# Performance work log

Measured on AMD Instinct MI355X. Metric: run time of the kernel, lower is better.

## Reference

```python
import jax, jax.numpy as jnp
import numpy as np

B, S, D = 64, 2048, 512


def setup_inputs() -> dict:
    key = jax.random.key(0)
    k1, k2, k3, k4 = jax.random.split(key, 4)
    decoder_output = jax.random.normal(k1, (B, 1, D), dtype=jnp.float32)
    encoder_output = jax.random.normal(k2, (B, S, D), dtype=jnp.float32)
    # W_a_tanh: Dense(D) applied to concat([dec, enc]) of width 2D
    scale_w = 1.0 / np.sqrt(2 * D)
    W_t = jax.random.normal(k3, (2 * D, D), dtype=jnp.float32) * scale_w
    b_t = jnp.zeros((D,), dtype=jnp.float32)
    # v_a: Dense(1)
    v_a = jax.random.normal(k4, (D, 1), dtype=jnp.float32) * (1.0 / np.sqrt(D))
    b_v = jnp.zeros((1,), dtype=jnp.float32)
    return {
        "decoder_output": decoder_output,
        "encoder_output": encoder_output,
        "W_t": W_t,
        "b_t": b_t,
        "v_a": v_a,
        "b_v": b_v,
    }


def reference(decoder_output, encoder_output, W_t, b_t, v_a, b_v):
    # concat-variant Luong attention
    dec = jnp.broadcast_to(decoder_output, encoder_output.shape)       # [B,S,D]
    concated = jnp.concatenate((dec, encoder_output), axis=-1)          # [B,S,2D]
    hidden = jnp.tanh(jnp.einsum('bse,ed->bsd', concated, W_t) + b_t)   # [B,S,D]
    score = (jnp.einsum('bsd,do->bso', hidden, v_a) + b_v)              # [B,S,1]
    score = jnp.transpose(score, (0, 2, 1))                             # [B,1,S]
    alignment_vector = jax.nn.softmax(score, axis=2)                    # [B,1,S]
    context_vector = jnp.matmul(alignment_vector, encoder_output)       # [B,1,D]
    return (context_vector, alignment_vector)
```

## Files before the change

### kernel.cpp

```cpp
#include <hip/hip_runtime.h>
#include <hip/hip_bf16.h>

#define BB 64
#define SS 2048
#define DD 512
#define MM (BB * SS)

typedef __attribute__((ext_vector_type(8))) short bf16x8;
typedef __attribute__((ext_vector_type(4))) float f32x4;

__device__ __forceinline__ unsigned f2bf(float f) {
    unsigned u = __float_as_uint(f);
    u += 0x7FFFu + ((u >> 16) & 1u);
    return u >> 16;
}

__device__ __forceinline__ float fast_tanh(float x) {
    float ax = fabsf(x);
    float e = __expf(-2.0f * ax);
    float t = (1.0f - e) * __builtin_amdgcn_rcpf(1.0f + e);
    return x < 0.0f ? -t : t;
}

__global__ void prep_w(const float* __restrict__ W, short* __restrict__ Bt) {
    __shared__ float tile[64][65];
    int kt = blockIdx.x >> 3;
    int nt = blockIdx.x & 7;
    int t = threadIdx.x;
    int c = t & 63;
    int rbase = (t >> 6) * 16;
    #pragma unroll
    for (int i = 0; i < 16; ++i) {
        int r = rbase + i;
        tile[r][c] = W[(size_t)(512 + kt * 64 + r) * DD + nt * 64 + c];
    }
    __syncthreads();
    #pragma unroll
    for (int i = 0; i < 16; ++i) {
        int r = rbase + i;
        Bt[(size_t)(nt * 64 + r) * DD + kt * 64 + c] = (short)f2bf(tile[c][r]);
    }
}

__global__ void prep_p(const float* __restrict__ dec, const float* __restrict__ W,
                       const float* __restrict__ bt, float* __restrict__ p) {
    int b = blockIdx.x;
    int d = blockIdx.y * 256 + threadIdx.x;
    float acc = bt[d];
    const float* dv = dec + (size_t)b * DD;
    #pragma unroll 8
    for (int e = 0; e < DD; ++e)
        acc += dv[e] * W[(size_t)e * DD + d];
    p[(size_t)b * DD + d] = acc;
}

__global__ __launch_bounds__(256, 2)
void score_gemm(const float* __restrict__ enc,
                const short* __restrict__ Bt,
                const float* __restrict__ p,
                const float* __restrict__ va,
                float* __restrict__ score) {
    __shared__ short Alds[2][128 * 32];
    __shared__ short Blds[2][128 * 32];
    __shared__ float sp[4][64];

    const int tid  = threadIdx.x;
    const int wave = tid >> 6;
    const int lane = tid & 63;
    const int mblk = blockIdx.x >> 2;
    const int n0   = (blockIdx.x & 3) * 128;
    const int m0   = mblk * 128;

    const int wm = wave >> 1, wn = wave & 1;
    const int lm = lane & 15, lq = lane >> 4;

    f32x4 acc[4][4];
    #pragma unroll
    for (int i = 0; i < 4; ++i)
        #pragma unroll
        for (int j = 0; j < 4; ++j)
            acc[i][j] = (f32x4){0.f, 0.f, 0.f, 0.f};

    const int arow = tid >> 1;
    const int acol = (tid & 1) * 16;
    const float* aptr = enc + (size_t)(m0 + arow) * DD + acol;

    const short* bptr = Bt + (size_t)(n0 + wave * 32 + (lane >> 2)) * DD + (lane & 3) * 8;

    #pragma unroll
    for (int i = 0; i < 2; ++i)
        __builtin_amdgcn_global_load_lds(
            (const __attribute__((address_space(1))) void*)(bptr + (size_t)i * 16 * DD),
            (__attribute__((address_space(3))) void*)(&Blds[0][(wave * 32 + i * 16) * 32]),
            16, 0, 0);
    {
        f32x4 x0 = *(const f32x4*)(aptr);
        f32x4 x1 = *(const f32x4*)(aptr + 4);
        f32x4 x2 = *(const f32x4*)(aptr + 8);
        f32x4 x3 = *(const f32x4*)(aptr + 12);
        int4 p0, p1;
        p0.x = f2bf(x0.x) | (f2bf(x0.y) << 16);
        p0.y = f2bf(x0.z) | (f2bf(x0.w) << 16);
        p0.z = f2bf(x1.x) | (f2bf(x1.y) << 16);
        p0.w = f2bf(x1.z) | (f2bf(x1.w) << 16);
        p1.x = f2bf(x2.x) | (f2bf(x2.y) << 16);
        p1.y = f2bf(x2.z) | (f2bf(x2.w) << 16);
        p1.z = f2bf(x3.x) | (f2bf(x3.y) << 16);
        p1.w = f2bf(x3.z) | (f2bf(x3.w) << 16);
        *(int4*)(&Alds[0][arow * 32 + acol]) = p0;
        *(int4*)(&Alds[0][arow * 32 + acol + 8]) = p1;
    }
    __syncthreads();

    for (int kt = 0; kt < 16; ++kt) {
        const int c = kt & 1;
        const bool pf = kt < 15;
        f32x4 x0, x1, x2, x3;
        if (pf) {
            const int kn = (kt + 1) * 32;
            #pragma unroll
            for (int i = 0; i < 2; ++i)
                __builtin_amdgcn_global_load_lds(
                    (const __attribute__((address_space(1))) void*)(bptr + (size_t)i * 16 * DD + kn),
                    (__attribute__((address_space(3))) void*)(&Blds[1 - c][(wave * 32 + i * 16) * 32]),
                    16, 0, 0);
            x0 = *(const f32x4*)(aptr + kn);
            x1 = *(const f32x4*)(aptr + kn + 4);
            x2 = *(const f32x4*)(aptr + kn + 8);
            x3 = *(const f32x4*)(aptr + kn + 12);
        }
        bf16x8 af[4];
        #pragma unroll
        for (int mf = 0; mf < 4; ++mf)
            af[mf] = *(const bf16x8*)(&Alds[c][(wm * 64 + mf * 16 + lm) * 32 + lq * 8]);
        #pragma unroll
        for (int nf = 0; nf < 4; ++nf) {
            bf16x8 bfr = *(const bf16x8*)(&Blds[c][(wn * 64 + nf * 16 + lm) * 32 + lq * 8]);
            #pragma unroll
            for (int mf = 0; mf < 4; ++mf)
                acc[mf][nf] = __builtin_amdgcn_mfma_f32_16x16x32_bf16(af[mf], bfr, acc[mf][nf], 0, 0, 0);
        }
        if (pf) {
            int4 p0, p1;
            p0.x = f2bf(x0.x) | (f2bf(x0.y) << 16);
            p0.y = f2bf(x0.z) | (f2bf(x0.w) << 16);
            p0.z = f2bf(x1.x) | (f2bf(x1.y) << 16);
            p0.w = f2bf(x1.z) | (f2bf(x1.w) << 16);
            p1.x = f2bf(x2.x) | (f2bf(x2.y) << 16);
            p1.y = f2bf(x2.z) | (f2bf(x2.w) << 16);
            p1.z = f2bf(x3.x) | (f2bf(x3.y) << 16);
            p1.w = f2bf(x3.z) | (f2bf(x3.w) << 16);
            *(int4*)(&Alds[1 - c][arow * 32 + acol]) = p0;
            *(int4*)(&Alds[1 - c][arow * 32 + acol + 8]) = p1;
        }
        __syncthreads();
    }

    const int b = m0 >> 11;
    float rowsum[4][4];
    #pragma unroll
    for (int mf = 0; mf < 4; ++mf)
        #pragma unroll
        for (int r = 0; r < 4; ++r) rowsum[mf][r] = 0.f;

    #pragma unroll
    for (int nf = 0; nf < 4; ++nf) {
        int n = n0 + wn * 64 + nf * 16 + lm;
        float pv = p[(size_t)b * DD + n];
        float vv = va[n];
        #pragma unroll
        for (int mf = 0; mf < 4; ++mf)
            #pragma unroll
            for (int r = 0; r < 4; ++r)
                rowsum[mf][r] += fast_tanh(pv + acc[mf][nf][r]) * vv;
    }
    #pragma unroll
    for (int mf = 0; mf < 4; ++mf)
        #pragma unroll
        for (int r = 0; r < 4; ++r) {
            float s = rowsum[mf][r];
            s += __shfl_xor(s, 1);
            s += __shfl_xor(s, 2);
            s += __shfl_xor(s, 4);
            s += __shfl_xor(s, 8);
            rowsum[mf][r] = s;
        }
    if (lm == 0) {
        #pragma unroll
        for (int mf = 0; mf < 4; ++mf)
            #pragma unroll
            for (int r = 0; r < 4; ++r)
                sp[wave][mf * 16 + lq * 4 + r] = rowsum[mf][r];
    }
    __syncthreads();
    if (tid < 128) {
        int row = tid & 63, half = tid >> 6;
        float v = sp[half * 2][row] + sp[half * 2 + 1][row];
        atomicAdd(&score[(size_t)m0 + half * 64 + row], v);
    }
}

__global__ void softmax_k(const float* __restrict__ score, float* __restrict__ align) {
    __shared__ float red[256];
    int b = blockIdx.x, tid = threadIdx.x;
    const float* s = score + (size_t)b * SS;
    float vals[8];
    float mx = -1e30f;
    #pragma unroll
    for (int i = 0; i < 8; ++i) {
        vals[i] = s[i * 256 + tid];
        mx = fmaxf(mx, vals[i]);
    }
    red[tid] = mx; __syncthreads();
    for (int off = 128; off > 0; off >>= 1) {
        if (tid < off) red[tid] = fmaxf(red[tid], red[tid + off]);
        __syncthreads();
    }
    mx = red[0]; __syncthreads();
    float sum = 0.f;
    #pragma unroll
    for (int i = 0; i < 8; ++i) {
        vals[i] = __expf(vals[i] - mx);
        sum += vals[i];
    }
    red[tid] = sum; __syncthreads();
    for (int off = 128; off > 0; off >>= 1) {
        if (tid < off) red[tid] += red[tid + off];
        __syncthreads();
    }
    float inv = 1.0f / red[0];
    #pragma unroll
    for (int i = 0; i < 8; ++i)
        align[(size_t)b * SS + i * 256 + tid] = vals[i] * inv;
}

__global__ void context_k(const float* __restrict__ enc, const float* __restrict__ align,
                          float* __restrict__ ctx) {
    int bx = blockIdx.x;
    int b = bx >> 4, chunk = bx & 15;
    int tid = threadIdx.x;
    const float2* e2 = (const float2*)(enc + ((size_t)b * SS + chunk * 128) * DD);
    const float* a = align + (size_t)b * SS + chunk * 128;
    float2 acc = {0.f, 0.f};
    #pragma unroll 4
    for (int s = 0; s < 128; ++s) {
        float av = a[s];
        float2 e = e2[(size_t)s * 256 + tid];
        acc.x += av * e.x;
        acc.y += av * e.y;
    }
    atomicAdd(&ctx[(size_t)b * DD + tid * 2], acc.x);
    atomicAdd(&ctx[(size_t)b * DD + tid * 2 + 1], acc.y);
}

extern "C" void kernel_launch(void* const* d_in, const int* in_sizes, int n_in,
                              void* d_out, int out_size, void* d_ws, size_t ws_size,
                              hipStream_t stream) {
    const float* dec = (const float*)d_in[0];
    const float* enc = (const float*)d_in[1];
    const float* W   = (const float*)d_in[2];
    const float* bt  = (const float*)d_in[3];
    const float* va  = (const float*)d_in[4];

    float* out   = (float*)d_out;
    float* ctx   = out;
    float* align = out + BB * DD;

    char*  ws    = (char*)d_ws;
    short* Bt    = (short*)ws;
    float* p     = (float*)(ws + 512 * 512 * 2);
    float* score = (float*)(ws + 512 * 512 * 2 + BB * DD * 4);

    hipMemsetAsync(ctx, 0, BB * DD * sizeof(float), stream);
    hipMemsetAsync(score, 0, MM * sizeof(float), stream);
    prep_w<<<64, 256, 0, stream>>>(W, Bt);
    prep_p<<<dim3(BB, 2), 256, 0, stream>>>(dec, W, bt, p);
    score_gemm<<<MM / 32, 256, 0, stream>>>(enc, Bt, p, va, score);
    softmax_k<<<BB, 256, 0, stream>>>(score, align);
    context_k<<<BB * 16, 256, 0, stream>>>(enc, align, ctx);
}
```

Measured before the change: 538.0 us.

## Pre-convert encoder to bf16 and stream both GEMM operands via direct LDS loads

Adds a separate pass that converts the fp32 encoder output to bf16 in workspace. The score GEMM then loads both A and B tiles with global_load_lds double buffering instead of per-thread fp32 loads, conversion and LDS stores, and raises the occupancy hint to 4 blocks per CU. The trade is an extra full read of the fp32 encoder plus a bf16 write and re-read (about 128 MB of extra traffic) in exchange for a leaner GEMM main loop. It also needs a large workspace, with a fallback to the old fp32 kernel when the workspace is too small.

```diff
diff --git a/kernel.cpp b/kernel.cpp
--- a/kernel.cpp
+++ b/kernel.cpp
@@ -20,6 +20,18 @@
     float e = __expf(-2.0f * ax);
     float t = (1.0f - e) * __builtin_amdgcn_rcpf(1.0f + e);
     return x < 0.0f ? -t : t;
+}
+
+__global__ void cvt_enc(const float* __restrict__ enc, short* __restrict__ enc16) {
+    size_t i = ((size_t)blockIdx.x * 256 + threadIdx.x) * 8;
+    f32x4 a = *(const f32x4*)(enc + i);
+    f32x4 b = *(const f32x4*)(enc + i + 4);
+    int4 pk;
+    pk.x = f2bf(a.x) | (f2bf(a.y) << 16);
+    pk.y = f2bf(a.z) | (f2bf(a.w) << 16);
+    pk.z = f2bf(b.x) | (f2bf(b.y) << 16);
+    pk.w = f2bf(b.z) | (f2bf(b.w) << 16);
+    *(int4*)(enc16 + i) = pk;
 }
 
 __global__ void prep_w(const float* __restrict__ W, short* __restrict__ Bt) {
@@ -54,8 +66,8 @@
     p[(size_t)b * DD + d] = acc;
 }
 
-__global__ __launch_bounds__(256, 2)
-void score_gemm(const float* __restrict__ enc,
+__global__ __launch_bounds__(256, 4)
+void score_gemm(const short* __restrict__ enc16,
                 const short* __restrict__ Bt,
                 const float* __restrict__ p,
                 const float* __restrict__ va,
@@ -81,10 +93,126 @@
         for (int j = 0; j < 4; ++j)
             acc[i][j] = (f32x4){0.f, 0.f, 0.f, 0.f};
 
+    const short* aptr = enc16 + (size_t)(m0 + wave * 32 + (lane >> 2)) * DD + (lane & 3) * 8;
+    const short* bptr = Bt    + (size_t)(n0 + wave * 32 + (lane >> 2)) * DD + (lane & 3) * 8;
+
+    #pragma unroll
+    for (int i = 0; i < 2; ++i) {
+        __builtin_amdgcn_global_load_lds(
+            (const __attribute__((address_space(1))) void*)(aptr + (size_t)i * 16 * DD),
+            (__attribute__((address_space(3))) void*)(&Alds[0][(wave * 32 + i * 16) * 32]),
+            16, 0, 0);
+        __builtin_amdgcn_global_load_lds(
+            (const __attribute__((address_space(1))) void*)(bptr + (size_t)i * 16 * DD),
+            (__attribute__((address_space(3))) void*)(&Blds[0][(wave * 32 + i * 16) * 32]),
+            16, 0, 0);
+    }
+    __syncthreads();
+
+    for (int kt = 0; kt < 16; ++kt) {
+        const int c = kt & 1;
+        if (kt < 15) {
+            const int kn = (kt + 1) * 32;
+            #pragma unroll
+            for (int i = 0; i < 2; ++i) {
+                __builtin_amdgcn_global_load_lds(
+                    (const __attribute__((address_space(1))) void*)(aptr + (size_t)i * 16 * DD + kn),
+                    (__attribute__((address_space(3))) void*)(&Alds[1 - c][(wave * 32 + i * 16) * 32]),
+                    16, 0, 0);
+                __builtin_amdgcn_global_load_lds(
+                    (const __attribute__((address_space(1))) void*)(bptr + (size_t)i * 16 * DD + kn),
+                    (__attribute__((address_space(3))) void*)(&Blds[1 - c][(wave * 32 + i * 16) * 32]),
+                    16, 0, 0);
+            }
+        }
+        bf16x8 af[4];
+        #pragma unroll
+        for (int mf = 0; mf < 4; ++mf)
+            af[mf] = *(const bf16x8*)(&Alds[c][(wm * 64 + mf * 16 + lm) * 32 + lq * 8]);
+        #pragma unroll
+        for (int nf = 0; nf < 4; ++nf) {
+            bf16x8 bfr = *(const bf16x8*)(&Blds[c][(wn * 64 + nf * 16 + lm) * 32 + lq * 8]);
+            #pragma unroll
+            for (int mf = 0; mf < 4; ++mf)
+                acc[mf][nf] = __builtin_amdgcn_mfma_f32_16x16x32_bf16(af[mf], bfr, acc[mf][nf], 0, 0, 0);
+        }
+        __syncthreads();
+    }
+
+    const int b = m0 >> 11;
+    float rowsum[4][4];
+    #pragma unroll
+    for (int mf = 0; mf < 4; ++mf)
+        #pragma unroll
+        for (int r = 0; r < 4; ++r) rowsum[mf][r] = 0.f;
+
+    #pragma unroll
+    for (int nf = 0; nf < 4; ++nf) {
+        int n = n0 + wn * 64 + nf * 16 + lm;
+        float pv = p[(size_t)b * DD + n];
+        float vv = va[n];
+        #pragma unroll
+        for (int mf = 0; mf < 4; ++mf)
+            #pragma unroll
+            for (int r = 0; r < 4; ++r)
+                rowsum[mf][r] += fast_tanh(pv + acc[mf][nf][r]) * vv;
+    }
+    #pragma unroll
+    for (int mf = 0; mf < 4; ++mf)
+        #pragma unroll
+        for (int r = 0; r < 4; ++r) {
+            float s = rowsum[mf][r];
+            s += __shfl_xor(s, 1);
+            s += __shfl_xor(s, 2);
+            s += __shfl_xor(s, 4);
+            s += __shfl_xor(s, 8);
+            rowsum[mf][r] = s;
+        }
+    if (lm == 0) {
+        #pragma unroll
+        for (int mf = 0; mf < 4; ++mf)
+            #pragma unroll
+            for (int r = 0; r < 4; ++r)
+                sp[wave][mf * 16 + lq * 4 + r] = rowsum[mf][r];
+    }
+    __syncthreads();
+    if (tid < 128) {
+        int row = tid & 63, half = tid >> 6;
+        float v = sp[half * 2][row] + sp[half * 2 + 1][row];
+        atomicAdd(&score[(size_t)m0 + half * 64 + row], v);
+    }
+}
+
+__global__ __launch_bounds__(256, 2)
+void score_gemm_f32(const float* __restrict__ enc,
+                    const short* __restrict__ Bt,
+                    const float* __restrict__ p,
+                    const float* __restrict__ va,
+                    float* __restrict__ score) {
+    __shared__ short Alds[2][128 * 32];
+    __shared__ short Blds[2][128 * 32];
+    __shared__ float sp[4][64];
+
+    const int tid  = threadIdx.x;
+    const int wave = tid >> 6;
+    const int lane = tid & 63;
+    const int mblk = blockIdx.x >> 2;
+    const int n0   = (blockIdx.x & 3) * 128;
+    const int m0   = mblk * 128;
+
+    const int wm = wave >> 1, wn = wave & 1;
+    const int lm = lane & 15, lq = lane >> 4;
+
+    f32x4 acc[4][4];
+    #pragma unroll
+    for (int i = 0; i < 4; ++i)
+        #pragma unroll
+        for (int j = 0; j < 4; ++j)
+            acc[i][j] = (f32x4){0.f, 0.f, 0.f, 0.f};
+
     const int arow = tid >> 1;
     const int acol = (tid & 1) * 16;
     const float* aptr = enc + (size_t)(m0 + arow) * DD + acol;
-
     const short* bptr = Bt + (size_t)(n0 + wave * 32 + (lane >> 2)) * DD + (lane & 3) * 8;
 
     #pragma unroll
@@ -266,16 +394,35 @@
     float* ctx   = out;
     float* align = out + BB * DD;
 
-    char*  ws    = (char*)d_ws;
-    short* Bt    = (short*)ws;
-    float* p     = (float*)(ws + 512 * 512 * 2);
-    float* score = (float*)(ws + 512 * 512 * 2 + BB * DD * 4);
-
-    hipMemsetAsync(ctx, 0, BB * DD * sizeof(float), stream);
-    hipMemsetAsync(score, 0, MM * sizeof(float), stream);
-    prep_w<<<64, 256, 0, stream>>>(W, Bt);
-    prep_p<<<dim3(BB, 2), 256, 0, stream>>>(dec, W, bt, p);
-    score_gemm<<<MM / 32, 256, 0, stream>>>(enc, Bt, p, va, score);
-    softmax_k<<<BB, 256, 0, stream>>>(score, align);
-    context_k<<<BB * 16, 256, 0, stream>>>(enc, align, ctx);
-}
+    const size_t enc16_bytes = (size_t)MM * DD * 2;
+    const size_t small_bytes = 512 * 1024 + 128 * 1024 + 512 * 1024;
+    char* ws = (char*)d_ws;
+
+    if (ws_size >= enc16_bytes + small_bytes) {
+        short* enc16 = (short*)ws;
+        short* Bt    = (short*)(ws + enc16_bytes);
+        float* p     = (float*)(ws + enc16_bytes + 512 * 1024);
+        float* score = (float*)(ws + enc16_bytes + 512 * 1024 + 128 * 1024);
+
+        hipMemsetAsync(ctx, 0, BB * DD * sizeof(float), stream);
+        hipMemsetAsync(score, 0, MM * sizeof(float), stream);
+        cvt_enc<<<(MM * DD) / (256 * 8), 256, 0, stream>>>(enc, enc16);
+        prep_w<<<64, 256, 0, stream>>>(W, Bt);
+        prep_p<<<dim3(BB, 2), 256, 0, stream>>>(dec, W, bt, p);
+        score_gemm<<<MM / 32, 256, 0, stream>>>(enc16, Bt, p, va, score);
+        softmax_k<<<BB, 256, 0, stream>>>(score, align);
+        context_k<<<BB * 16, 256, 0, stream>>>(enc, align, ctx);
+    } else {
+        short* Bt    = (short*)ws;
+        float* p     = (float*)(ws + 512 * 1024);
+        float* score = (float*)(ws + 512 * 1024 + 128 * 1024);
+
+        hipMemsetAsync(ctx, 0, BB * DD * sizeof(float), stream);
+        hipMemsetAsync(score, 0, MM * sizeof(float), stream);
+        prep_w<<<64, 256, 0, stream>>>(W, Bt);
+        prep_p<<<dim3(BB, 2), 256, 0, stream>>>(dec, W, bt, p);
+        score_gemm_f32<<<MM / 32, 256, 0, stream>>>(enc, Bt, p, va, score);
+        softmax_k<<<BB, 256, 0, stream>>>(score, align);
+        context_k<<<BB * 16, 256, 0, stream>>>(enc, align, ctx);
+    }
+}
```

New measurement: 584.2 us. 8.6% more time.
